# Optimization experiments

Hardware: AMD Instinct MI355X
Metric: run time of the kernel (lower is better)

Reference implementation:

```python
import jax, jax.numpy as jnp
import numpy as np

EPS = 1e-4

def softmax_kernel(data, proj, is_query):
    # FAVOR+ positive softmax random features; data: [b,h,l,d], proj: [d,m]
    d = data.shape[-1]
    m = proj.shape[-1]
    data_normalizer = d ** -0.25  # normalize_data=True
    ratio = m ** -0.5
    data_dash = jnp.einsum('bhld,dm->bhlm', data, proj) * data_normalizer
    diag = 0.5 * jnp.sum(data * data, axis=-1, keepdims=True) * (data_normalizer ** 2)
    if is_query:
        stab = jnp.max(data_dash, axis=-1, keepdims=True)   # per-token max
    else:
        stab = jnp.max(data_dash, axis=(-2, -1), keepdims=True)  # per (b,h) max
    out = ratio * (jnp.exp(data_dash - diag - stab) + EPS)
    return out, stab

def low_mem_attn(qp, kp, v, causal, chunk):
    # qp,kp: [b,h,l,m] positive features; v: [b,h,l,d]
    b, h, l, m = qp.shape
    d = v.shape[-1]
    if not causal:
        kv = jnp.einsum('bhlm,bhld->bhmd', kp, v)
        den = jnp.einsum('bhlm,bhm->bhl', qp, jnp.sum(kp, axis=2))
        return jnp.einsum('bhlm,bhmd->bhld', qp, kv) / den[..., None]
    nc = l // chunk
    qc = qp.reshape(b, h, nc, chunk, m)
    kc = kp.reshape(b, h, nc, chunk, m)
    vc = v.reshape(b, h, nc, chunk, d)
    # intra-chunk causal part
    mask = jnp.tril(jnp.ones((chunk, chunk), dtype=qp.dtype))
    scores = jnp.einsum('bhcim,bhcjm->bhcij', qc, kc) * mask
    intra = jnp.einsum('bhcij,bhcjd->bhcid', scores, vc)
    intra_den = jnp.sum(scores, axis=-1)  # [b,h,nc,chunk]
    # inter-chunk via exclusive cumulative sums of KV state
    kv = jnp.einsum('bhcjm,bhcjd->bhcmd', kc, vc)          # per-chunk KV
    kv_prev = jnp.cumsum(kv, axis=2) - kv                   # exclusive cumsum
    ks = jnp.sum(kc, axis=3)                                # [b,h,nc,m]
    ks_prev = jnp.cumsum(ks, axis=2) - ks
    inter = jnp.einsum('bhcim,bhcmd->bhcid', qc, kv_prev)
    inter_den = jnp.einsum('bhcim,bhcm->bhci', qc, ks_prev)
    out = (intra + inter) / (intra_den + inter_den)[..., None]
    return out.reshape(b, h, l, d)


def setup_inputs() -> dict:
    key = jax.random.key(0)
    k1, k2, k3, k4 = jax.random.split(key, 4)
    B, H, L, D, M = 2, 16, 4096, 64, 64
    return {
        'q': jax.random.normal(k1, (B, H, L, D), dtype=jnp.float32),
        'k': jax.random.normal(k2, (B, H, L, D), dtype=jnp.float32),
        'v': jax.random.normal(k3, (B, H, L, D), dtype=jnp.float32),
        'projection_matrix': jax.random.normal(k4, (D, M), dtype=jnp.float32),
        'chunk_size': 128,
    }


def reference(q, k, v, projection_matrix, chunk_size):
    qp, _ = softmax_kernel(q, projection_matrix, is_query=True)
    kp, _key_maxima = softmax_kernel(k, projection_matrix, is_query=False)
    o = low_mem_attn(qp, kp, v, causal=True, chunk=chunk_size)
    return o
```

## Files before the change

### kernel.cpp

```cpp
#include <hip/hip_runtime.h>
#include <hip/hip_bf16.h>

#define TPB 256
#define ATPB 512

constexpr int   Bc = 2, Hc = 16, Lc = 4096, Dc = 64, Mc = 64, CHc = 128;
constexpr int   NCc = Lc / CHc;
constexpr int   BHc = Bc * Hc;
constexpr float DNF    = 0.35355339059327373f;
constexpr float RATIOF = 0.125f;
constexpr float EPSF   = 1e-4f;

constexpr long QP_OFF  = 0;
constexpr long KPB_OFF = 4194304;
constexpr long VTB_OFF = 8388608;
constexpr long KV_OFF  = 12582912;
constexpr long KVB_OFF = 16777216;
constexpr long KS_OFF  = 18874368;
constexpr long HM_OFF  = 18939904;

typedef __attribute__((ext_vector_type(8))) short bf16x8;
typedef __attribute__((ext_vector_type(4))) float f32x4;

__device__ __forceinline__ unsigned fordmap(float f) {
  unsigned u = __float_as_uint(f);
  return (u & 0x80000000u) ? ~u : (u | 0x80000000u);
}
__device__ __forceinline__ float fordunmap(unsigned u) {
  return __uint_as_float((u & 0x80000000u) ? (u & 0x7fffffffu) : ~u);
}
__device__ __forceinline__ unsigned pk2(float a, float b) {
  union { __hip_bfloat16 h; unsigned short u; } ca, cb;
  ca.h = __float2bfloat16(a); cb.h = __float2bfloat16(b);
  return ((unsigned)cb.u << 16) | (unsigned)ca.u;
}
__device__ __forceinline__ short f2bf(float a) {
  union { __hip_bfloat16 h; short s; } c; c.h = __float2bfloat16(a); return c.s;
}
__device__ __forceinline__ float bf2f(short s) {
  return __uint_as_float(((unsigned)(unsigned short)s) << 16);
}

__global__ void k_init(unsigned* hmax) {
  int t = threadIdx.x;
  if (t < BHc) hmax[t] = 0u;
}

__global__ __launch_bounds__(TPB) void k_featq(const float* __restrict__ x,
                                               const float* __restrict__ P,
                                               short* __restrict__ outb) {
  __shared__ short xb[128 * 72];
  __shared__ short Pt[64 * 72];
  __shared__ short ob[128 * 64];
  __shared__ float diag_s[128];
  const int t = threadIdx.x;
  const long rowbase = (long)blockIdx.x * 128;
  for (int i = t; i < 4096; i += TPB) {
    const int r = i >> 5, d2 = (i & 31) * 2;
    float2 xv = *(const float2*)&x[rowbase * 64 + r * 64 + d2];
    *(unsigned*)&xb[r * 72 + d2] = pk2(xv.x, xv.y);
  }
  for (int i = t; i < 4096; i += TPB) {
    const int d = i >> 6, m = i & 63;
    Pt[m * 72 + d] = f2bf(P[i]);
  }
  {
    const int row = t >> 1, half = t & 1;
    float s = 0.f;
#pragma unroll
    for (int d = 0; d < 32; d += 4) {
      float4 vv = *(const float4*)&x[(rowbase + row) * 64 + half * 32 + d];
      s += vv.x * vv.x + vv.y * vv.y + vv.z * vv.z + vv.w * vv.w;
    }
    s += __shfl_xor(s, 1);
    if (half == 0) diag_s[row] = 0.0625f * s;
  }
  __syncthreads();

  const int w = t >> 6, lane = t & 63;
  const int lrow = lane & 15, quad = lane >> 4;
#pragma unroll
  for (int rt2 = 0; rt2 < 2; ++rt2) {
    const int rt = w * 2 + rt2;
    const bf16x8 a0 = *(const bf16x8*)&xb[(rt * 16 + lrow) * 72 + quad * 8];
    const bf16x8 a1 = *(const bf16x8*)&xb[(rt * 16 + lrow) * 72 + 32 + quad * 8];
    f32x4 c[4];
#pragma unroll
    for (int ct = 0; ct < 4; ++ct) {
      const bf16x8 b0 = *(const bf16x8*)&Pt[(ct * 16 + lrow) * 72 + quad * 8];
      const bf16x8 b1 = *(const bf16x8*)&Pt[(ct * 16 + lrow) * 72 + 32 + quad * 8];
      f32x4 cc = {0.f, 0.f, 0.f, 0.f};
      cc = __builtin_amdgcn_mfma_f32_16x16x32_bf16(a0, b0, cc, 0, 0, 0);
      cc = __builtin_amdgcn_mfma_f32_16x16x32_bf16(a1, b1, cc, 0, 0, 0);
#pragma unroll
      for (int r = 0; r < 4; ++r) cc[r] *= DNF;
      c[ct] = cc;
    }
#pragma unroll
    for (int r = 0; r < 4; ++r) {
      float mx = fmaxf(fmaxf(c[0][r], c[1][r]), fmaxf(c[2][r], c[3][r]));
#pragma unroll
      for (int off = 1; off < 16; off <<= 1) mx = fmaxf(mx, __shfl_xor(mx, off));
      const int row = rt * 16 + quad * 4 + r;
      const float dg = diag_s[row];
#pragma unroll
      for (int ct = 0; ct < 4; ++ct)
        ob[row * 64 + ct * 16 + lrow] =
            f2bf(RATIOF * (expf(c[ct][r] - dg - mx) + EPSF));
    }
  }
  __syncthreads();
  for (int i = t; i < 1024; i += TPB)
    *(uint4*)&outb[rowbase * 64 + i * 8] = *(const uint4*)&ob[i * 8];
}

__global__ __launch_bounds__(TPB) void k_stab(const float* __restrict__ kin,
                                              const float* __restrict__ P,
                                              unsigned* __restrict__ hmax) {
  __shared__ short kb[128 * 72];
  __shared__ short Pt[64 * 72];
  __shared__ unsigned bmax_s;
  const int t = threadIdx.x;
  const long base = (long)blockIdx.x * 8192;
  if (t == 0) bmax_s = 0u;
  for (int i = t; i < 4096; i += TPB) {
    const int r = i >> 5, d2 = (i & 31) * 2;
    float2 kk = *(const float2*)&kin[base + r * 64 + d2];
    *(unsigned*)&kb[r * 72 + d2] = pk2(kk.x, kk.y);
  }
  for (int i = t; i < 4096; i += TPB) {
    const int d = i >> 6, m = i & 63;
    Pt[m * 72 + d] = f2bf(P[i]);
  }
  __syncthreads();
  const int w = t >> 6, lane = t & 63;
  const int lrow = lane & 15, quad = lane >> 4;
  float tmax = -1e30f;
#pragma unroll
  for (int rt2 = 0; rt2 < 2; ++rt2) {
    const int rt = w * 2 + rt2;
    const bf16x8 a0 = *(const bf16x8*)&kb[(rt * 16 + lrow) * 72 + quad * 8];
    const bf16x8 a1 = *(const bf16x8*)&kb[(rt * 16 + lrow) * 72 + 32 + quad * 8];
#pragma unroll
    for (int ct = 0; ct < 4; ++ct) {
      const bf16x8 b0 = *(const bf16x8*)&Pt[(ct * 16 + lrow) * 72 + quad * 8];
      const bf16x8 b1 = *(const bf16x8*)&Pt[(ct * 16 + lrow) * 72 + 32 + quad * 8];
      f32x4 cc = {0.f, 0.f, 0.f, 0.f};
      cc = __builtin_amdgcn_mfma_f32_16x16x32_bf16(a0, b0, cc, 0, 0, 0);
      cc = __builtin_amdgcn_mfma_f32_16x16x32_bf16(a1, b1, cc, 0, 0, 0);
#pragma unroll
      for (int r = 0; r < 4; ++r) tmax = fmaxf(tmax, cc[r] * DNF);
    }
  }
#pragma unroll
  for (int off = 1; off < 64; off <<= 1) tmax = fmaxf(tmax, __shfl_xor(tmax, off));
  if (lane == 0) atomicMax(&bmax_s, fordmap(tmax));
  __syncthreads();
  if (t == 0) atomicMax(&hmax[blockIdx.x >> 5], bmax_s);
}

__global__ __launch_bounds__(TPB) void k_kv(const float* __restrict__ kin,
                                            const float* __restrict__ v,
                                            const float* __restrict__ P,
                                            float* __restrict__ kvT,
                                            float* __restrict__ ks,
                                            short* __restrict__ kpb,
                                            short* __restrict__ vtb,
                                            const unsigned* __restrict__ hmax) {
  __shared__ short kb[128 * 72];
  __shared__ short Pt[64 * 72];
  __shared__ short Kt[64 * 136];
  __shared__ short Vt[64 * 136];
  __shared__ float diag_s[128];
  __shared__ float ks_s[64];
  const int t = threadIdx.x;
  const int bhc = blockIdx.x;
  const long base = (long)bhc * 8192;
  const float stab = fordunmap(hmax[bhc >> 5]);
  if (t < 64) ks_s[t] = 0.f;
  for (int i = t; i < 4096; i += TPB) {
    const int r = i >> 5, d2 = (i & 31) * 2;
    float2 kk = *(const float2*)&kin[base + r * 64 + d2];
    *(unsigned*)&kb[r * 72 + d2] = pk2(kk.x, kk.y);
  }
  for (int i = t; i < 4096; i += TPB) {
    const int d = i >> 6, m = i & 63;
    Pt[m * 72 + d] = f2bf(P[i]);
  }
  {
    const int d2 = (t & 31) * 2;
    for (int i = t; i < 4096; i += TPB) {
      const int j = i >> 5;
      float2 vv = *(const float2*)&v[base + j * 64 + d2];
      Vt[d2 * 136 + j] = f2bf(vv.x);
      Vt[(d2 + 1) * 136 + j] = f2bf(vv.y);
    }
  }
  {
    const int row = t >> 1, half = t & 1;
    float s = 0.f;
#pragma unroll
    for (int d = 0; d < 32; d += 4) {
      float4 vv = *(const float4*)&kin[base + row * 64 + half * 32 + d];
      s += vv.x * vv.x + vv.y * vv.y + vv.z * vv.z + vv.w * vv.w;
    }
    s += __shfl_xor(s, 1);
    if (half == 0) diag_s[row] = 0.0625f * s;
  }
  __syncthreads();
  for (int i = t; i < 1024; i += TPB) {
    const int d = i >> 4, c8 = (i & 15) * 8;
    *(uint4*)&vtb[base + d * 128 + c8] = *(const uint4*)&Vt[d * 136 + c8];
  }
  const int w = t >> 6, lane = t & 63;
  const int lrow = lane & 15, quad = lane >> 4;
  float ksp_[4] = {0.f, 0.f, 0.f, 0.f};
#pragma unroll
  for (int rt2 = 0; rt2 < 2; ++rt2) {
    const int rt = w * 2 + rt2;
    const bf16x8 a0 = *(const bf16x8*)&kb[(rt * 16 + lrow) * 72 + quad * 8];
    const bf16x8 a1 = *(const bf16x8*)&kb[(rt * 16 + lrow) * 72 + 32 + quad * 8];
#pragma unroll
    for (int ct = 0; ct < 4; ++ct) {
      const bf16x8 b0 = *(const bf16x8*)&Pt[(ct * 16 + lrow) * 72 + quad * 8];
      const bf16x8 b1 = *(const bf16x8*)&Pt[(ct * 16 + lrow) * 72 + 32 + quad * 8];
      f32x4 cc = {0.f, 0.f, 0.f, 0.f};
      cc = __builtin_amdgcn_mfma_f32_16x16x32_bf16(a0, b0, cc, 0, 0, 0);
      cc = __builtin_amdgcn_mfma_f32_16x16x32_bf16(a1, b1, cc, 0, 0, 0);
      const int m = ct * 16 + lrow;
#pragma unroll
      for (int r = 0; r < 4; ++r) {
        const int row = rt * 16 + quad * 4 + r;
        const float e = RATIOF * (expf(cc[r] * DNF - diag_s[row] - stab) + EPSF);
        Kt[m * 136 + row] = f2bf(e);
        ksp_[ct] += e;
      }
    }
  }
#pragma unroll
  for (int ct = 0; ct < 4; ++ct) {
    ksp_[ct] += __shfl_xor(ksp_[ct], 16);
    ksp_[ct] += __shfl_xor(ksp_[ct], 32);
  }
  if (quad == 0) {
#pragma unroll
    for (int ct = 0; ct < 4; ++ct) atomicAdd(&ks_s[ct * 16 + lrow], ksp_[ct]);
  }
  __syncthreads();
  if (t < 64) ks[bhc * 64 + t] = ks_s[t];
  for (int i = t; i < 1024; i += TPB) {
    const int j = i >> 3, m8 = (i & 7) * 8;
    unsigned u[4];
#pragma unroll
    for (int p = 0; p < 4; ++p) {
      const unsigned lo = (unsigned short)Kt[(m8 + 2 * p) * 136 + j];
      const unsigned hi = (unsigned short)Kt[(m8 + 2 * p + 1) * 136 + j];
      u[p] = lo | (hi << 16);
    }
    uint4 w4; w4.x = u[0]; w4.y = u[1]; w4.z = u[2]; w4.w = u[3];
    *(uint4*)&kpb[base + j * 64 + m8] = w4;
  }
  f32x4 acc[4];
#pragma unroll
  for (int mt = 0; mt < 4; ++mt) acc[mt] = (f32x4){0.f, 0.f, 0.f, 0.f};
#pragma unroll
  for (int ksq = 0; ksq < 4; ++ksq) {
    const bf16x8 a = *(const bf16x8*)&Vt[(w * 16 + lrow) * 136 + ksq * 32 + quad * 8];
#pragma unroll
    for (int mt = 0; mt < 4; ++mt) {
      const bf16x8 b = *(const bf16x8*)&Kt[(mt * 16 + lrow) * 136 + ksq * 32 + quad * 8];
      acc[mt] = __builtin_amdgcn_mfma_f32_16x16x32_bf16(a, b, acc[mt], 0, 0, 0);
    }
  }
  const long kvo = (long)bhc * 4096;
#pragma unroll
  for (int mt = 0; mt < 4; ++mt)
#pragma unroll
    for (int r = 0; r < 4; ++r)
      kvT[kvo + (long)(w * 16 + quad * 4 + r) * 64 + mt * 16 + lrow] = acc[mt][r];
}

__global__ void k_scan(const float* __restrict__ kv, short* __restrict__ kvb,
                       float* __restrict__ ks) {
  if (blockIdx.x < 512) {
    const int tid = blockIdx.x * TPB + threadIdx.x;
    const int bh = tid >> 12, rem = tid & 4095;
    float run = 0.f;
    for (int c = 0; c < NCc; ++c) {
      const long idx = ((long)(bh * NCc + c)) * 4096 + rem;
      kvb[idx] = f2bf(run);
      run += kv[idx];
    }
  } else {
    for (int tid = threadIdx.x; tid < BHc * 64; tid += TPB) {
      const int bh = tid >> 6, m = tid & 63;
      float run = 0.f;
      for (int c = 0; c < NCc; ++c) {
        const int idx = (bh * NCc + c) * 64 + m;
        const float val = ks[idx];
        ks[idx] = run;
        run += val;
      }
    }
  }
}

__global__ __launch_bounds__(ATPB, 4) void k_attn(const short* __restrict__ qpb,
                                                  const short* __restrict__ kpb,
                                                  const short* __restrict__ vtb,
                                                  const short* __restrict__ kvb,
                                                  const float* __restrict__ ksp,
                                                  float* __restrict__ outp) {
  __shared__ short Ks[128 * 72];
  __shared__ short Vt[64 * 136];
  __shared__ short KVt[64 * 72];
  __shared__ short Ps[128 * 136];
  __shared__ float kss[64];
  __shared__ float dens[128];
  const int t = threadIdx.x;
  const int bhc = blockIdx.x;
  const long cbase = (long)bhc * 8192;

  for (int i = t; i < 1024; i += ATPB) {
    const int r = i >> 3, c8 = (i & 7) * 8;
    *(uint4*)&Ks[r * 72 + c8] = *(const uint4*)&kpb[cbase + r * 64 + c8];
  }
  for (int i = t; i < 1024; i += ATPB) {
    const int d = i >> 4, c8 = (i & 15) * 8;
    *(uint4*)&Vt[d * 136 + c8] = *(const uint4*)&vtb[cbase + d * 128 + c8];
  }
  {
    const int d = t >> 3, c8 = (t & 7) * 8;
    *(uint4*)&KVt[d * 72 + c8] = *(const uint4*)&kvb[(long)bhc * 4096 + d * 64 + c8];
  }
  if (t < 64) kss[t] = ksp[bhc * 64 + t];
  for (int i = t; i < 1024; i += ATPB) {
    const int tp = i >> 8, rr = (i >> 4) & 15, cc = i & 15;
    Ps[(tp * 32 + rr) * 136 + tp * 32 + 16 + cc] = 0;
  }
  const int w = t >> 6, lane = t & 63;
  const int lrow = lane & 15, quad = lane >> 4;
  const int ri = w;
  const long qrb = cbase + (long)(ri * 16 + lrow) * 64;
  const bf16x8 a0 = *(const bf16x8*)&qpb[qrb + quad * 8];
  const bf16x8 a1 = *(const bf16x8*)&qpb[qrb + 32 + quad * 8];
  __syncthreads();

  float qks = 0.f;
#pragma unroll
  for (int j = 0; j < 8; ++j) {
    qks += bf2f(a0[j]) * kss[quad * 8 + j];
    qks += bf2f(a1[j]) * kss[32 + quad * 8 + j];
  }
  qks += __shfl_xor(qks, 16);
  qks += __shfl_xor(qks, 32);
  if (quad == 0) dens[ri * 16 + lrow] = qks;

  float rs0 = 0.f, rs1 = 0.f, rs2 = 0.f, rs3 = 0.f;
  for (int cj = 0; cj <= ri; ++cj) {
    const bf16x8 b0 = *(const bf16x8*)&Ks[(cj * 16 + lrow) * 72 + quad * 8];
    const bf16x8 b1 = *(const bf16x8*)&Ks[(cj * 16 + lrow) * 72 + 32 + quad * 8];
    f32x4 c = {0.f, 0.f, 0.f, 0.f};
    c = __builtin_amdgcn_mfma_f32_16x16x32_bf16(a0, b0, c, 0, 0, 0);
    c = __builtin_amdgcn_mfma_f32_16x16x32_bf16(a1, b1, c, 0, 0, 0);
    if (cj == ri) {
#pragma unroll
      for (int r = 0; r < 4; ++r)
        if (lrow > quad * 4 + r) c[r] = 0.f;
    }
    const int colb = cj * 16 + lrow;
    Ps[(ri * 16 + quad * 4 + 0) * 136 + colb] = f2bf(c[0]); rs0 += c[0];
    Ps[(ri * 16 + quad * 4 + 1) * 136 + colb] = f2bf(c[1]); rs1 += c[1];
    Ps[(ri * 16 + quad * 4 + 2) * 136 + colb] = f2bf(c[2]); rs2 += c[2];
    Ps[(ri * 16 + quad * 4 + 3) * 136 + colb] = f2bf(c[3]); rs3 += c[3];
  }
#pragma unroll
  for (int off = 1; off < 16; off <<= 1) {
    rs0 += __shfl_xor(rs0, off);
    rs1 += __shfl_xor(rs1, off);
    rs2 += __shfl_xor(rs2, off);
    rs3 += __shfl_xor(rs3, off);
  }
  if (lrow == 0) {
    dens[ri * 16 + quad * 4 + 0] += rs0;
    dens[ri * 16 + quad * 4 + 1] += rs1;
    dens[ri * 16 + quad * 4 + 2] += rs2;
    dens[ri * 16 + quad * 4 + 3] += rs3;
  }

  f32x4 acc0 = {0.f,0.f,0.f,0.f}, acc1 = {0.f,0.f,0.f,0.f};
  f32x4 acc2 = {0.f,0.f,0.f,0.f}, acc3 = {0.f,0.f,0.f,0.f};
  const int nj = (ri + 2) >> 1;
  for (int jc = 0; jc < nj; ++jc) {
    const bf16x8 a  = *(const bf16x8*)&Ps[(ri * 16 + lrow) * 136 + jc * 32 + quad * 8];
    const bf16x8 b0 = *(const bf16x8*)&Vt[(lrow) * 136 + jc * 32 + quad * 8];
    const bf16x8 b1 = *(const bf16x8*)&Vt[(16 + lrow) * 136 + jc * 32 + quad * 8];
    const bf16x8 b2 = *(const bf16x8*)&Vt[(32 + lrow) * 136 + jc * 32 + quad * 8];
    const bf16x8 b3 = *(const bf16x8*)&Vt[(48 + lrow) * 136 + jc * 32 + quad * 8];
    acc0 = __builtin_amdgcn_mfma_f32_16x16x32_bf16(a, b0, acc0, 0, 0, 0);
    acc1 = __builtin_amdgcn_mfma_f32_16x16x32_bf16(a, b1, acc1, 0, 0, 0);
    acc2 = __builtin_amdgcn_mfma_f32_16x16x32_bf16(a, b2, acc2, 0, 0, 0);
    acc3 = __builtin_amdgcn_mfma_f32_16x16x32_bf16(a, b3, acc3, 0, 0, 0);
  }
  {
    const bf16x8 b0 = *(const bf16x8*)&KVt[(lrow) * 72 + quad * 8];
    const bf16x8 b1 = *(const bf16x8*)&KVt[(16 + lrow) * 72 + quad * 8];
    const bf16x8 b2 = *(const bf16x8*)&KVt[(32 + lrow) * 72 + quad * 8];
    const bf16x8 b3 = *(const bf16x8*)&KVt[(48 + lrow) * 72 + quad * 8];
    acc0 = __builtin_amdgcn_mfma_f32_16x16x32_bf16(a0, b0, acc0, 0, 0, 0);
    acc1 = __builtin_amdgcn_mfma_f32_16x16x32_bf16(a0, b1, acc1, 0, 0, 0);
    acc2 = __builtin_amdgcn_mfma_f32_16x16x32_bf16(a0, b2, acc2, 0, 0, 0);
    acc3 = __builtin_amdgcn_mfma_f32_16x16x32_bf16(a0, b3, acc3, 0, 0, 0);
    const bf16x8 c0 = *(const bf16x8*)&KVt[(lrow) * 72 + 32 + quad * 8];
    const bf16x8 c1 = *(const bf16x8*)&KVt[(16 + lrow) * 72 + 32 + quad * 8];
    const bf16x8 c2 = *(const bf16x8*)&KVt[(32 + lrow) * 72 + 32 + quad * 8];
    const bf16x8 c3 = *(const bf16x8*)&KVt[(48 + lrow) * 72 + 32 + quad * 8];
    acc0 = __builtin_amdgcn_mfma_f32_16x16x32_bf16(a1, c0, acc0, 0, 0, 0);
    acc1 = __builtin_amdgcn_mfma_f32_16x16x32_bf16(a1, c1, acc1, 0, 0, 0);
    acc2 = __builtin_amdgcn_mfma_f32_16x16x32_bf16(a1, c2, acc2, 0, 0, 0);
    acc3 = __builtin_amdgcn_mfma_f32_16x16x32_bf16(a1, c3, acc3, 0, 0, 0);
  }
#pragma unroll
  for (int r = 0; r < 4; ++r) {
    const int row = ri * 16 + quad * 4 + r;
    const float inv = 1.f / dens[row];
    const long ob = cbase + (long)row * 64 + lrow;
    outp[ob]      = acc0[r] * inv;
    outp[ob + 16] = acc1[r] * inv;
    outp[ob + 32] = acc2[r] * inv;
    outp[ob + 48] = acc3[r] * inv;
  }
}

extern "C" void kernel_launch(void* const* d_in, const int* in_sizes, int n_in,
                              void* d_out, int out_size, void* d_ws, size_t ws_size,
                              hipStream_t stream) {
  const float* q = (const float*)d_in[0];
  const float* k = (const float*)d_in[1];
  const float* v = (const float*)d_in[2];
  const float* P = (const float*)d_in[3];
  float* ws = (float*)d_ws;
  short*    qpb  = (short*)(ws + QP_OFF);
  short*    kpb  = (short*)(ws + KPB_OFF);
  short*    vtb  = (short*)(ws + VTB_OFF);
  float*    kvT  = ws + KV_OFF;
  short*    kvb  = (short*)(ws + KVB_OFF);
  float*    ks   = ws + KS_OFF;
  unsigned* hmax = (unsigned*)(ws + HM_OFF);
  float* out = (float*)d_out;

  k_init<<<1, 64, 0, stream>>>(hmax);
  k_featq<<<dim3(1024), dim3(TPB), 0, stream>>>(q, P, qpb);
  k_stab<<<dim3(1024), dim3(TPB), 0, stream>>>(k, P, hmax);
  k_kv<<<dim3(1024), dim3(TPB), 0, stream>>>(k, v, P, kvT, ks, kpb, vtb, hmax);
  k_scan<<<dim3(513), dim3(TPB), 0, stream>>>(kvT, kvb, ks);
  k_attn<<<dim3(1024), dim3(ATPB), 0, stream>>>(qpb, kpb, vtb, kvb, ks, out);
}
```

Measured before the change: 210.0 us.

## Merge query-feature and key-max kernels, drop transposed V buffer

Combines the query feature-map kernel and the key stabilizer max kernel into one 2048-block launch that branches on block index. The kernel that zeroes the max buffer is replaced with a memset. The kv kernel no longer writes a transposed bf16 copy of V to workspace. Instead, the attention kernel reads fp32 V directly and transposes and packs it into shared memory. This cuts launch count and one global round trip for V, at the cost of wider fp32 reads and strided scalar loads in the attention kernel.

```diff
diff --git a/kernel.cpp b/kernel.cpp
--- a/kernel.cpp
+++ b/kernel.cpp
@@ -13,11 +13,10 @@
 
 constexpr long QP_OFF  = 0;
 constexpr long KPB_OFF = 4194304;
-constexpr long VTB_OFF = 8388608;
-constexpr long KV_OFF  = 12582912;
-constexpr long KVB_OFF = 16777216;
-constexpr long KS_OFF  = 18874368;
-constexpr long HM_OFF  = 18939904;
+constexpr long KV_OFF  = 8388608;
+constexpr long KVB_OFF = 12582912;
+constexpr long KS_OFF  = 14680064;
+constexpr long HM_OFF  = 14745600;
 
 typedef __attribute__((ext_vector_type(8))) short bf16x8;
 typedef __attribute__((ext_vector_type(4))) float f32x4;
@@ -41,20 +40,21 @@
   return __uint_as_float(((unsigned)(unsigned short)s) << 16);
 }
 
-__global__ void k_init(unsigned* hmax) {
-  int t = threadIdx.x;
-  if (t < BHc) hmax[t] = 0u;
-}
-
-__global__ __launch_bounds__(TPB) void k_featq(const float* __restrict__ x,
-                                               const float* __restrict__ P,
-                                               short* __restrict__ outb) {
+__global__ __launch_bounds__(TPB) void k_fs(const float* __restrict__ q,
+                                            const float* __restrict__ kin,
+                                            const float* __restrict__ P,
+                                            short* __restrict__ qpb,
+                                            unsigned* __restrict__ hmax) {
   __shared__ short xb[128 * 72];
   __shared__ short Pt[64 * 72];
   __shared__ short ob[128 * 64];
   __shared__ float diag_s[128];
+  __shared__ unsigned bmax_s;
   const int t = threadIdx.x;
-  const long rowbase = (long)blockIdx.x * 128;
+  const bool isq = blockIdx.x < 1024;
+  const int cb = isq ? blockIdx.x : (blockIdx.x - 1024);
+  const float* __restrict__ x = isq ? q : kin;
+  const long rowbase = (long)cb * 128;
   for (int i = t; i < 4096; i += TPB) {
     const int r = i >> 5, d2 = (i & 31) * 2;
     float2 xv = *(const float2*)&x[rowbase * 64 + r * 64 + d2];
@@ -64,7 +64,8 @@
     const int d = i >> 6, m = i & 63;
     Pt[m * 72 + d] = f2bf(P[i]);
   }
-  {
+  if (t == 0) bmax_s = 0u;
+  if (isq) {
     const int row = t >> 1, half = t & 1;
     float s = 0.f;
 #pragma unroll
@@ -79,6 +80,7 @@
 
   const int w = t >> 6, lane = t & 63;
   const int lrow = lane & 15, quad = lane >> 4;
+  float tmax = -1e30f;
 #pragma unroll
   for (int rt2 = 0; rt2 < 2; ++rt2) {
     const int rt = w * 2 + rt2;
@@ -96,67 +98,38 @@
       for (int r = 0; r < 4; ++r) cc[r] *= DNF;
       c[ct] = cc;
     }
-#pragma unroll
-    for (int r = 0; r < 4; ++r) {
-      float mx = fmaxf(fmaxf(c[0][r], c[1][r]), fmaxf(c[2][r], c[3][r]));
-#pragma unroll
-      for (int off = 1; off < 16; off <<= 1) mx = fmaxf(mx, __shfl_xor(mx, off));
-      const int row = rt * 16 + quad * 4 + r;
-      const float dg = diag_s[row];
+    if (isq) {
+#pragma unroll
+      for (int r = 0; r < 4; ++r) {
+        float mx = fmaxf(fmaxf(c[0][r], c[1][r]), fmaxf(c[2][r], c[3][r]));
+#pragma unroll
+        for (int off = 1; off < 16; off <<= 1) mx = fmaxf(mx, __shfl_xor(mx, off));
+        const int row = rt * 16 + quad * 4 + r;
+        const float dg = diag_s[row];
+#pragma unroll
+        for (int ct = 0; ct < 4; ++ct)
+          ob[row * 64 + ct * 16 + lrow] =
+              f2bf(RATIOF * (expf(c[ct][r] - dg - mx) + EPSF));
+      }
+    } else {
 #pragma unroll
       for (int ct = 0; ct < 4; ++ct)
-        ob[row * 64 + ct * 16 + lrow] =
-            f2bf(RATIOF * (expf(c[ct][r] - dg - mx) + EPSF));
-    }
+#pragma unroll
+        for (int r = 0; r < 4; ++r) tmax = fmaxf(tmax, c[ct][r]);
+    }
+  }
+  if (!isq) {
+#pragma unroll
+    for (int off = 1; off < 64; off <<= 1) tmax = fmaxf(tmax, __shfl_xor(tmax, off));
+    if (lane == 0) atomicMax(&bmax_s, fordmap(tmax));
   }
   __syncthreads();
-  for (int i = t; i < 1024; i += TPB)
-    *(uint4*)&outb[rowbase * 64 + i * 8] = *(const uint4*)&ob[i * 8];
-}
-
-__global__ __launch_bounds__(TPB) void k_stab(const float* __restrict__ kin,
-                                              const float* __restrict__ P,
-                                              unsigned* __restrict__ hmax) {
-  __shared__ short kb[128 * 72];
-  __shared__ short Pt[64 * 72];
-  __shared__ unsigned bmax_s;
-  const int t = threadIdx.x;
-  const long base = (long)blockIdx.x * 8192;
-  if (t == 0) bmax_s = 0u;
-  for (int i = t; i < 4096; i += TPB) {
-    const int r = i >> 5, d2 = (i & 31) * 2;
-    float2 kk = *(const float2*)&kin[base + r * 64 + d2];
-    *(unsigned*)&kb[r * 72 + d2] = pk2(kk.x, kk.y);
-  }
-  for (int i = t; i < 4096; i += TPB) {
-    const int d = i >> 6, m = i & 63;
-    Pt[m * 72 + d] = f2bf(P[i]);
-  }
-  __syncthreads();
-  const int w = t >> 6, lane = t & 63;
-  const int lrow = lane & 15, quad = lane >> 4;
-  float tmax = -1e30f;
-#pragma unroll
-  for (int rt2 = 0; rt2 < 2; ++rt2) {
-    const int rt = w * 2 + rt2;
-    const bf16x8 a0 = *(const bf16x8*)&kb[(rt * 16 + lrow) * 72 + quad * 8];
-    const bf16x8 a1 = *(const bf16x8*)&kb[(rt * 16 + lrow) * 72 + 32 + quad * 8];
-#pragma unroll
-    for (int ct = 0; ct < 4; ++ct) {
-      const bf16x8 b0 = *(const bf16x8*)&Pt[(ct * 16 + lrow) * 72 + quad * 8];
-      const bf16x8 b1 = *(const bf16x8*)&Pt[(ct * 16 + lrow) * 72 + 32 + quad * 8];
-      f32x4 cc = {0.f, 0.f, 0.f, 0.f};
-      cc = __builtin_amdgcn_mfma_f32_16x16x32_bf16(a0, b0, cc, 0, 0, 0);
-      cc = __builtin_amdgcn_mfma_f32_16x16x32_bf16(a1, b1, cc, 0, 0, 0);
-#pragma unroll
-      for (int r = 0; r < 4; ++r) tmax = fmaxf(tmax, cc[r] * DNF);
-    }
-  }
-#pragma unroll
-  for (int off = 1; off < 64; off <<= 1) tmax = fmaxf(tmax, __shfl_xor(tmax, off));
-  if (lane == 0) atomicMax(&bmax_s, fordmap(tmax));
-  __syncthreads();
-  if (t == 0) atomicMax(&hmax[blockIdx.x >> 5], bmax_s);
+  if (isq) {
+    for (int i = t; i < 1024; i += TPB)
+      *(uint4*)&qpb[rowbase * 64 + i * 8] = *(const uint4*)&ob[i * 8];
+  } else {
+    if (t == 0) atomicMax(&hmax[cb >> 5], bmax_s);
+  }
 }
 
 __global__ __launch_bounds__(TPB) void k_kv(const float* __restrict__ kin,
@@ -165,7 +138,6 @@
                                             float* __restrict__ kvT,
                                             float* __restrict__ ks,
                                             short* __restrict__ kpb,
-                                            short* __restrict__ vtb,
                                             const unsigned* __restrict__ hmax) {
   __shared__ short kb[128 * 72];
   __shared__ short Pt[64 * 72];
@@ -208,10 +180,6 @@
     if (half == 0) diag_s[row] = 0.0625f * s;
   }
   __syncthreads();
-  for (int i = t; i < 1024; i += TPB) {
-    const int d = i >> 4, c8 = (i & 15) * 8;
-    *(uint4*)&vtb[base + d * 128 + c8] = *(const uint4*)&Vt[d * 136 + c8];
-  }
   const int w = t >> 6, lane = t & 63;
   const int lrow = lane & 15, quad = lane >> 4;
   float ksp_[4] = {0.f, 0.f, 0.f, 0.f};
@@ -307,7 +275,7 @@
 
 __global__ __launch_bounds__(ATPB, 4) void k_attn(const short* __restrict__ qpb,
                                                   const short* __restrict__ kpb,
-                                                  const short* __restrict__ vtb,
+                                                  const float* __restrict__ v,
                                                   const short* __restrict__ kvb,
                                                   const float* __restrict__ ksp,
                                                   float* __restrict__ outp) {
@@ -325,9 +293,11 @@
     const int r = i >> 3, c8 = (i & 7) * 8;
     *(uint4*)&Ks[r * 72 + c8] = *(const uint4*)&kpb[cbase + r * 64 + c8];
   }
-  for (int i = t; i < 1024; i += ATPB) {
-    const int d = i >> 4, c8 = (i & 15) * 8;
-    *(uint4*)&Vt[d * 136 + c8] = *(const uint4*)&vtb[cbase + d * 128 + c8];
+  for (int i = t; i < 4096; i += ATPB) {
+    const int jp = i >> 6, d = i & 63;
+    const float a = v[cbase + (2 * jp) * 64 + d];
+    const float b = v[cbase + (2 * jp + 1) * 64 + d];
+    *(unsigned*)&Vt[d * 136 + 2 * jp] = pk2(a, b);
   }
   {
     const int d = t >> 3, c8 = (t & 7) * 8;
@@ -442,17 +412,15 @@
   float* ws = (float*)d_ws;
   short*    qpb  = (short*)(ws + QP_OFF);
   short*    kpb  = (short*)(ws + KPB_OFF);
-  short*    vtb  = (short*)(ws + VTB_OFF);
   float*    kvT  = ws + KV_OFF;
   short*    kvb  = (short*)(ws + KVB_OFF);
   float*    ks   = ws + KS_OFF;
   unsigned* hmax = (unsigned*)(ws + HM_OFF);
   float* out = (float*)d_out;
 
-  k_init<<<1, 64, 0, stream>>>(hmax);
-  k_featq<<<dim3(1024), dim3(TPB), 0, stream>>>(q, P, qpb);
-  k_stab<<<dim3(1024), dim3(TPB), 0, stream>>>(k, P, hmax);
-  k_kv<<<dim3(1024), dim3(TPB), 0, stream>>>(k, v, P, kvT, ks, kpb, vtb, hmax);
+  hipMemsetAsync(hmax, 0, BHc * sizeof(unsigned), stream);
+  k_fs<<<dim3(2048), dim3(TPB), 0, stream>>>(q, k, P, qpb, hmax);
+  k_kv<<<dim3(1024), dim3(TPB), 0, stream>>>(k, v, P, kvT, ks, kpb, hmax);
   k_scan<<<dim3(513), dim3(TPB), 0, stream>>>(kvT, kvb, ks);
-  k_attn<<<dim3(1024), dim3(ATPB), 0, stream>>>(qpb, kpb, vtb, kvb, ks, out);
-}
+  k_attn<<<dim3(1024), dim3(ATPB), 0, stream>>>(qpb, kpb, v, kvb, ks, out);
+}
```

New measurement: 203.7 us. 3.0% less time.
